# Performance work log

Measured on AMD Instinct MI355X. Metric: run time of the kernel, lower is better.

## Reference

```python
import jax, jax.numpy as jnp
import numpy as np

B, T, D, H, O = 64, 2048, 256, 256, 128


def setup_inputs() -> dict:
    key = jax.random.key(0)
    ks = jax.random.split(key, 12)
    s_in = 1.0 / np.sqrt(H)
    inp = {
        "x": jax.random.normal(ks[0], (B, T, D), dtype=jnp.float32),
        # layer 0 (input_dim -> hidden_dim)
        "W_ih0": jax.random.uniform(ks[1], (H, D), jnp.float32, -s_in, s_in),
        "W_hh0": jax.random.uniform(ks[2], (H, H), jnp.float32, -s_in, s_in),
        "b_ih0": jax.random.uniform(ks[3], (H,), jnp.float32, -s_in, s_in),
        "b_hh0": jax.random.uniform(ks[4], (H,), jnp.float32, -s_in, s_in),
        # layer 1 (hidden_dim -> hidden_dim)
        "W_ih1": jax.random.uniform(ks[5], (H, H), jnp.float32, -s_in, s_in),
        "W_hh1": jax.random.uniform(ks[6], (H, H), jnp.float32, -s_in, s_in),
        "b_ih1": jax.random.uniform(ks[7], (H,), jnp.float32, -s_in, s_in),
        "b_hh1": jax.random.uniform(ks[8], (H,), jnp.float32, -s_in, s_in),
        # final linear
        "fc_w": jax.random.uniform(ks[9], (O, H), jnp.float32, -s_in, s_in),
        "fc_b": jax.random.uniform(ks[10], (O,), jnp.float32, -s_in, s_in),
    }
    return inp


def _rnn_layer(x_tbd, W_ih, W_hh, b_ih, b_hh):
    """x_tbd: [T, B, D_in] -> [T, B, H]. h_t = relu(x_t W_ih^T + b_ih + h_{t-1} W_hh^T + b_hh)."""
    # precompute input projection for all timesteps (one big GEMM)
    xp = jnp.einsum('tbd,hd->tbh', x_tbd, W_ih) + (b_ih + b_hh)

    def step(h, xp_t):
        h = jax.nn.relu(xp_t + h @ W_hh.T)
        return h, h

    h0 = jnp.zeros((x_tbd.shape[1], W_hh.shape[0]), dtype=x_tbd.dtype)
    _, hs = jax.lax.scan(step, h0, xp)
    return hs


def reference(x, W_ih0, W_hh0, b_ih0, b_hh0, W_ih1, W_hh1, b_ih1, b_hh1, fc_w, fc_b):
    x_tbd = jnp.transpose(x, (1, 0, 2))           # [T, B, D]
    h1 = _rnn_layer(x_tbd, W_ih0, W_hh0, b_ih0, b_hh0)   # [T, B, H]
    h2 = _rnn_layer(h1, W_ih1, W_hh1, b_ih1, b_hh1)      # [T, B, H]
    last = h2[-1]                                  # out[:, -1, :] -> [B, H]
    return last @ fc_w.T + fc_b                    # [B, O]
```

## Files before the change

kernel.cpp:

```cpp
#include <hip/hip_runtime.h>
#include <hip/hip_bf16.h>
#include <stdint.h>


typedef float    f32x4  __attribute__((ext_vector_type(4)));
typedef short    s16x8  __attribute__((ext_vector_type(8)));
typedef uint32_t u32x2  __attribute__((ext_vector_type(2)));
typedef uint32_t u32x4v __attribute__((ext_vector_type(4)));

#define T_STEPS 2048

template<bool C, class A, class B> struct cond_ { using type = A; };
template<class A, class B> struct cond_<false, A, B> { using type = B; };

static __device__ __forceinline__ ushort f2bf(float f) {
  uint32_t u = __builtin_bit_cast(uint32_t, f);
  u += 0x7fffu + ((u >> 16) & 1u);
  return (ushort)(u >> 16);
}
static __device__ __forceinline__ float bf2f(ushort h) {
  return __builtin_bit_cast(float, (uint32_t)h << 16);
}
static __device__ __forceinline__ uint32_t packbf(float lo, float hi) {
  return (uint32_t)f2bf(lo) | ((uint32_t)f2bf(hi) << 16);
}
static __device__ __forceinline__ s16x8 pack8(float4 a, float4 b) {
  u32x4v u;
  u.x = packbf(a.x, a.y); u.y = packbf(a.z, a.w);
  u.z = packbf(b.x, b.y); u.w = packbf(b.z, b.w);
  return __builtin_bit_cast(s16x8, u);
}
struct hl2 { uint32_t hi, lo; };
static __device__ __forceinline__ hl2 split2(float a, float b) {
  const ushort ha = f2bf(a), hb = f2bf(b);
  const ushort la = f2bf(a - bf2f(ha)), lb = f2bf(b - bf2f(hb));
  hl2 r;
  r.hi = (uint32_t)ha | ((uint32_t)hb << 16);
  r.lo = (uint32_t)la | ((uint32_t)lb << 16);
  return r;
}
static __device__ __forceinline__ f32x4 expand16(u32x2 p) {
  f32x4 r;
  r.x = __builtin_bit_cast(float, p.x << 16);
  r.y = __builtin_bit_cast(float, p.x & 0xffff0000u);
  r.z = __builtin_bit_cast(float, p.y << 16);
  r.w = __builtin_bit_cast(float, p.y & 0xffff0000u);
  return r;
}
static __device__ __forceinline__ f32x4 acc_of(f32x4 v) { return v; }
static __device__ __forceinline__ f32x4 acc_of(u32x2 v) { return expand16(v); }

#define MFMA16(a, b, c) __builtin_amdgcn_mfma_f32_16x16x32_bf16((a), (b), (c), 0, 0, 0)

template<int MODE, bool XP16>
__global__ __launch_bounds__(256, 2)
void proj_kernel(const void* __restrict__ inp, const float* __restrict__ W,
                 const float* __restrict__ ba, const float* __restrict__ bb,
                 void* __restrict__ xp)
{
  const int tid = threadIdx.x;
  const int w = tid >> 6, lane = tid & 63, q = lane >> 4, r = lane & 15;

  s16x8 wf[4][8];
  float bs[4];
#pragma unroll
  for (int n = 0; n < 4; ++n) {
    const int j = 16 * (4 * w + n) + r;
    bs[n] = ba[j] + bb[j];
    const float* wr = W + (size_t)j * 256 + 8 * q;
#pragma unroll
    for (int c = 0; c < 8; ++c) {
      const float4 f0 = *(const float4*)(wr + 32 * c);
      const float4 f1 = *(const float4*)(wr + 32 * c + 4);
      wf[n][c] = pack8(f0, f1);
    }
  }

  const int t0 = blockIdx.x * 8;
  for (int tt = 0; tt < 8; ++tt) {
    const int t = t0 + tt;
    for (int bg = 0; bg < 4; ++bg) {
      s16x8 af[8];
      if (MODE == 1) {
        const unsigned char* hsl = (const unsigned char*)inp
            + (size_t)t * 32768 + (size_t)bg * 8192 + lane * 16;
#pragma unroll
        for (int c = 0; c < 8; ++c)
          af[c] = __builtin_bit_cast(s16x8, *(const u32x4v*)(hsl + c * 1024));
      } else {
        const float* arow = (const float*)inp + ((size_t)(16 * bg + r) * 2048 + t) * 256 + 8 * q;
#pragma unroll
        for (int c = 0; c < 8; ++c) {
          const float4 f0 = *(const float4*)(arow + 32 * c);
          const float4 f1 = *(const float4*)(arow + 32 * c + 4);
          af[c] = pack8(f0, f1);
        }
      }
      f32x4 a0 = {bs[0], bs[0], bs[0], bs[0]};
      f32x4 a1 = {bs[1], bs[1], bs[1], bs[1]};
      f32x4 a2 = {bs[2], bs[2], bs[2], bs[2]};
      f32x4 a3 = {bs[3], bs[3], bs[3], bs[3]};
#pragma unroll
      for (int c = 0; c < 8; ++c) {
        a0 = MFMA16(af[c], wf[0][c], a0);
        a1 = MFMA16(af[c], wf[1][c], a1);
        a2 = MFMA16(af[c], wf[2][c], a2);
        a3 = MFMA16(af[c], wf[3][c], a3);
      }
      const int ob = (t * 4 + bg) * 1024 + (4 * w) * 64 + lane;
      if constexpr (XP16) {
        u32x2* const xpo = (u32x2*)xp;
        u32x2 s0, s1, s2, s3;
        s0.x = packbf(a0.x, a0.y); s0.y = packbf(a0.z, a0.w);
        s1.x = packbf(a1.x, a1.y); s1.y = packbf(a1.z, a1.w);
        s2.x = packbf(a2.x, a2.y); s2.y = packbf(a2.z, a2.w);
        s3.x = packbf(a3.x, a3.y); s3.y = packbf(a3.z, a3.w);
        xpo[ob +   0] = s0;
        xpo[ob +  64] = s1;
        xpo[ob + 128] = s2;
        xpo[ob + 192] = s3;
      } else {
        f32x4* const xpo = (f32x4*)xp;
        xpo[ob +   0] = a0;
        xpo[ob +  64] = a1;
        xpo[ob + 128] = a2;
        xpo[ob + 192] = a3;
      }
    }
  }
}

template<int LAYER, bool XP16>
__global__ __launch_bounds__(256, 1)
void recur_kernel(const void* __restrict__ xp, const float* __restrict__ Whh,
                  char* __restrict__ h1out, const float* __restrict__ fcw,
                  const float* __restrict__ fcb, float* __restrict__ out)
{
  using XPT = typename cond_<XP16, u32x2, f32x4>::type;
  const int tid = threadIdx.x;
  const int w = tid >> 6, lane = tid & 63, q = lane >> 4, r = lane & 15;
  const int bg = blockIdx.x;

  __shared__ __align__(16) unsigned char smem[16384];

  s16x8 whi[4][8], wlo[4][8];
#pragma unroll
  for (int n = 0; n < 4; ++n) {
    const float* wr = Whh + (size_t)(16 * (4 * w + n) + r) * 256 + 8 * q;
#pragma unroll
    for (int c = 0; c < 8; ++c) {
      const float4 f0 = *(const float4*)(wr + 32 * c);
      const float4 f1 = *(const float4*)(wr + 32 * c + 4);
      const hl2 p0 = split2(f0.x, f0.y);
      const hl2 p1 = split2(f0.z, f0.w);
      const hl2 p2 = split2(f1.x, f1.y);
      const hl2 p3 = split2(f1.z, f1.w);
      u32x4v H, L;
      H.x = p0.hi; L.x = p0.lo;
      H.y = p1.hi; L.y = p1.lo;
      H.z = p2.hi; L.z = p2.lo;
      H.w = p3.hi; L.w = p3.lo;
      whi[n][c] = __builtin_bit_cast(s16x8, H);
      wlo[n][c] = __builtin_bit_cast(s16x8, L);
    }
  }

  {
    uint32_t* z = (uint32_t*)smem;
#pragma unroll
    for (int i = 0; i < 16; ++i) z[tid + 256 * i] = 0u;
  }
  __syncthreads();

  const XPT* __restrict__ xpv = (const XPT*)xp;
  const int xpbase = bg * 1024 + (4 * w) * 64 + lane;

  XPT pfA[4], pfB[4];
#pragma unroll
  for (int n = 0; n < 4; ++n) {
    pfA[n] = xpv[xpbase + n * 64];
    pfB[n] = xpv[4096 + xpbase + n * 64];
  }

  int rb[4];
#pragma unroll
  for (int n = 0; n < 4; ++n) {
    const int k0 = 64 * w + 16 * n + r;
    rb[n] = (k0 >> 5) * 1024 + ((k0 >> 3) & 3) * 256 + (4 * q) * 16 + (k0 & 7) * 2;
  }
  const int rdoff = lane * 16;

#define RSTEP(T_, RD_, WR_, PF_) do {                                           \
    u32x4v afr[8];                                                              \
    _Pragma("unroll")                                                           \
    for (int c = 0; c < 8; ++c)                                                 \
      afr[c] = *(const u32x4v*)(smem + (RD_) + c * 1024 + rdoff);               \
    if (LAYER == 0 && w == 0 && (T_) > 0) {                                     \
      char* hb = h1out + (size_t)((T_) - 1) * 32768 + (size_t)bg * 8192 + rdoff;\
      _Pragma("unroll")                                                         \
      for (int c = 0; c < 8; ++c) *(u32x4v*)(hb + c * 1024) = afr[c];           \
    }                                                                           \
    f32x4 ac0 = acc_of(PF_[0]), ac1 = acc_of(PF_[1]);                           \
    f32x4 ac2 = acc_of(PF_[2]), ac3 = acc_of(PF_[3]);                           \
    { int tp = (T_) + 2; if (tp > T_STEPS - 1) tp = T_STEPS - 1;                \
      const int xo = tp * 4096 + xpbase;                                        \
      PF_[0] = xpv[xo]; PF_[1] = xpv[xo + 64];                                  \
      PF_[2] = xpv[xo + 128]; PF_[3] = xpv[xo + 192]; }                         \
    _Pragma("unroll")                                                           \
    for (int c = 0; c < 8; ++c) {                                               \
      const s16x8 a = __builtin_bit_cast(s16x8, afr[c]);                        \
      ac0 = MFMA16(a, whi[0][c], ac0); ac1 = MFMA16(a, whi[1][c], ac1);         \
      ac2 = MFMA16(a, whi[2][c], ac2); ac3 = MFMA16(a, whi[3][c], ac3);         \
      ac0 = MFMA16(a, wlo[0][c], ac0); ac1 = MFMA16(a, wlo[1][c], ac1);         \
      ac2 = MFMA16(a, wlo[2][c], ac2); ac3 = MFMA16(a, wlo[3][c], ac3);         \
    }                                                                           \
    unsigned char* const wb = smem + (WR_);                                     \
    *(ushort*)(wb + rb[0] +  0) = f2bf(fmaxf(ac0.x, 0.f));                      \
    *(ushort*)(wb + rb[0] + 16) = f2bf(fmaxf(ac0.y, 0.f));                      \
    *(ushort*)(wb + rb[0] + 32) = f2bf(fmaxf(ac0.z, 0.f));                      \
    *(ushort*)(wb + rb[0] + 48) = f2bf(fmaxf(ac0.w, 0.f));                      \
    *(ushort*)(wb + rb[1] +  0) = f2bf(fmaxf(ac1.x, 0.f));                      \
    *(ushort*)(wb + rb[1] + 16) = f2bf(fmaxf(ac1.y, 0.f));                      \
    *(ushort*)(wb + rb[1] + 32) = f2bf(fmaxf(ac1.z, 0.f));                      \
    *(ushort*)(wb + rb[1] + 48) = f2bf(fmaxf(ac1.w, 0.f));                      \
    *(ushort*)(wb + rb[2] +  0) = f2bf(fmaxf(ac2.x, 0.f));                      \
    *(ushort*)(wb + rb[2] + 16) = f2bf(fmaxf(ac2.y, 0.f));                      \
    *(ushort*)(wb + rb[2] + 32) = f2bf(fmaxf(ac2.z, 0.f));                      \
    *(ushort*)(wb + rb[2] + 48) = f2bf(fmaxf(ac2.w, 0.f));                      \
    *(ushort*)(wb + rb[3] +  0) = f2bf(fmaxf(ac3.x, 0.f));                      \
    *(ushort*)(wb + rb[3] + 16) = f2bf(fmaxf(ac3.y, 0.f));                      \
    *(ushort*)(wb + rb[3] + 32) = f2bf(fmaxf(ac3.z, 0.f));                      \
    *(ushort*)(wb + rb[3] + 48) = f2bf(fmaxf(ac3.w, 0.f));                      \
    __syncthreads();                                                            \
  } while (0)

  for (int t = 0; t < T_STEPS; t += 2) {
    RSTEP(t,     0,    8192, pfA);
    RSTEP(t + 1, 8192, 0,    pfB);
  }
#undef RSTEP

  if (LAYER == 0 && w == 0) {
    char* hb = h1out + (size_t)2047 * 32768 + (size_t)bg * 8192 + rdoff;
#pragma unroll
    for (int c = 0; c < 8; ++c)
      *(u32x4v*)(hb + c * 1024) = *(const u32x4v*)(smem + c * 1024 + rdoff);
  }

  if (LAYER == 1) {
    const int m  = tid >> 4;
    const int og = tid & 15;
    float a8[8];
#pragma unroll
    for (int oo = 0; oo < 8; ++oo) a8[oo] = fcb[og * 8 + oo];
    for (int c = 0; c < 8; ++c) {
#pragma unroll
      for (int qq = 0; qq < 4; ++qq) {
        const u32x4v hv = *(const u32x4v*)(smem + c * 1024 + (16 * qq + m) * 16);
        float hf[8];
        hf[0] = bf2f((ushort)(hv.x & 0xffff)); hf[1] = bf2f((ushort)(hv.x >> 16));
        hf[2] = bf2f((ushort)(hv.y & 0xffff)); hf[3] = bf2f((ushort)(hv.y >> 16));
        hf[4] = bf2f((ushort)(hv.z & 0xffff)); hf[5] = bf2f((ushort)(hv.z >> 16));
        hf[6] = bf2f((ushort)(hv.w & 0xffff)); hf[7] = bf2f((ushort)(hv.w >> 16));
        const int kb = 32 * c + 8 * qq;
#pragma unroll
        for (int oo = 0; oo < 8; ++oo) {
          const float* fw = fcw + (size_t)(og * 8 + oo) * 256 + kb;
          const float4 g0 = *(const float4*)(fw);
          const float4 g1 = *(const float4*)(fw + 4);
          a8[oo] += hf[0] * g0.x + hf[1] * g0.y + hf[2] * g0.z + hf[3] * g0.w
                  + hf[4] * g1.x + hf[5] * g1.y + hf[6] * g1.z + hf[7] * g1.w;
        }
      }
    }
#pragma unroll
    for (int oo = 0; oo < 8; ++oo)
      out[(16 * bg + m) * 128 + og * 8 + oo] = a8[oo];
  }
}

extern "C" void kernel_launch(void* const* d_in, const int* in_sizes, int n_in,
                              void* d_out, int out_size, void* d_ws, size_t ws_size,
                              hipStream_t stream) {
  (void)in_sizes; (void)n_in; (void)out_size;
  const float* x     = (const float*)d_in[0];
  const float* W_ih0 = (const float*)d_in[1];
  const float* W_hh0 = (const float*)d_in[2];
  const float* b_ih0 = (const float*)d_in[3];
  const float* b_hh0 = (const float*)d_in[4];
  const float* W_ih1 = (const float*)d_in[5];
  const float* W_hh1 = (const float*)d_in[6];
  const float* b_ih1 = (const float*)d_in[7];
  const float* b_hh1 = (const float*)d_in[8];
  const float* fcw   = (const float*)d_in[9];
  const float* fcb   = (const float*)d_in[10];

  const bool big = ws_size >= (size_t)201326592;
  if (big) {
    void* xp = d_ws;
    char* h1 = (char*)d_ws + (size_t)134217728;
    proj_kernel<0, false><<<256, 256, 0, stream>>>(x, W_ih0, b_ih0, b_hh0, xp);
    recur_kernel<0, false><<<4, 256, 0, stream>>>(xp, W_hh0, h1, nullptr, nullptr, nullptr);
    proj_kernel<1, false><<<256, 256, 0, stream>>>(h1, W_ih1, b_ih1, b_hh1, xp);
    recur_kernel<1, false><<<4, 256, 0, stream>>>(xp, W_hh1, nullptr, fcw, fcb, (float*)d_out);
  } else {
    void* xp = d_ws;
    char* h1 = (char*)d_ws + (size_t)67108864;
    proj_kernel<0, true><<<256, 256, 0, stream>>>(x, W_ih0, b_ih0, b_hh0, xp);
    recur_kernel<0, true><<<4, 256, 0, stream>>>(xp, W_hh0, h1, nullptr, nullptr, nullptr);
    proj_kernel<1, true><<<256, 256, 0, stream>>>(h1, W_ih1, b_ih1, b_hh1, xp);
    recur_kernel<1, true><<<4, 256, 0, stream>>>(xp, W_hh1, nullptr, fcw, fcb, (float*)d_out);
  }
}
```

Baseline: 4.615 ms.

## Swap MFMA operand order so recurrent outputs store as packed bf16 vectors

Swaps the A and B operands of the MFMAs in both the projection and recurrent kernels. Each lane's accumulator then holds four consecutive hidden units for one batch row instead of four batch rows for one unit. In the recurrent step this lets each lane convert its outputs with the hardware packed bf16 convert and write them to LDS as four 8-byte stores, replacing sixteen 2-byte stores. The step sits on the serial critical path, so fewer LDS stores and conversions per step should help. The bias is now loaded per lane as a vector. The projection output layout changes as a consequence, so it must stay consistent with how the recurrent kernel reads xp.

```diff
diff --git a/kernel.cpp b/kernel.cpp
--- a/kernel.cpp
+++ b/kernel.cpp
@@ -23,6 +23,11 @@
 }
 static __device__ __forceinline__ uint32_t packbf(float lo, float hi) {
   return (uint32_t)f2bf(lo) | ((uint32_t)f2bf(hi) << 16);
+}
+static __device__ __forceinline__ uint32_t cvtpk(float lo, float hi) {
+  uint32_t d;
+  asm("v_cvt_pk_bf16_f32 %0, %1, %2" : "=v"(d) : "v"(lo), "v"(hi));
+  return d;
 }
 static __device__ __forceinline__ s16x8 pack8(float4 a, float4 b) {
   u32x4v u;
@@ -62,11 +67,15 @@
   const int w = tid >> 6, lane = tid & 63, q = lane >> 4, r = lane & 15;
 
   s16x8 wf[4][8];
-  float bs[4];
+  f32x4 bs4[4];
 #pragma unroll
   for (int n = 0; n < 4; ++n) {
+    const int j0 = 16 * (4 * w + n) + 4 * q;
+    const float4 b0 = *(const float4*)(ba + j0);
+    const float4 b1 = *(const float4*)(bb + j0);
+    bs4[n].x = b0.x + b1.x; bs4[n].y = b0.y + b1.y;
+    bs4[n].z = b0.z + b1.z; bs4[n].w = b0.w + b1.w;
     const int j = 16 * (4 * w + n) + r;
-    bs[n] = ba[j] + bb[j];
     const float* wr = W + (size_t)j * 256 + 8 * q;
 #pragma unroll
     for (int c = 0; c < 8; ++c) {
@@ -96,16 +105,16 @@
           af[c] = pack8(f0, f1);
         }
       }
-      f32x4 a0 = {bs[0], bs[0], bs[0], bs[0]};
-      f32x4 a1 = {bs[1], bs[1], bs[1], bs[1]};
-      f32x4 a2 = {bs[2], bs[2], bs[2], bs[2]};
-      f32x4 a3 = {bs[3], bs[3], bs[3], bs[3]};
+      f32x4 a0 = bs4[0];
+      f32x4 a1 = bs4[1];
+      f32x4 a2 = bs4[2];
+      f32x4 a3 = bs4[3];
 #pragma unroll
       for (int c = 0; c < 8; ++c) {
-        a0 = MFMA16(af[c], wf[0][c], a0);
-        a1 = MFMA16(af[c], wf[1][c], a1);
-        a2 = MFMA16(af[c], wf[2][c], a2);
-        a3 = MFMA16(af[c], wf[3][c], a3);
+        a0 = MFMA16(wf[0][c], af[c], a0);
+        a1 = MFMA16(wf[1][c], af[c], a1);
+        a2 = MFMA16(wf[2][c], af[c], a2);
+        a3 = MFMA16(wf[3][c], af[c], a3);
       }
       const int ob = (t * 4 + bg) * 1024 + (4 * w) * 64 + lane;
       if constexpr (XP16) {
@@ -182,11 +191,11 @@
     pfB[n] = xpv[4096 + xpbase + n * 64];
   }
 
-  int rb[4];
-#pragma unroll
-  for (int n = 0; n < 4; ++n) {
-    const int k0 = 64 * w + 16 * n + r;
-    rb[n] = (k0 >> 5) * 1024 + ((k0 >> 3) & 3) * 256 + (4 * q) * 16 + (k0 & 7) * 2;
+  int wrb[4];
+#pragma unroll
+  for (int nt = 0; nt < 4; ++nt) {
+    const int k0 = 64 * w + 16 * nt + 4 * q;
+    wrb[nt] = (k0 >> 5) * 1024 + ((k0 >> 3) & 3) * 256 + r * 16 + (k0 & 7) * 2;
   }
   const int rdoff = lane * 16;
 
@@ -209,28 +218,26 @@
     _Pragma("unroll")                                                           \
     for (int c = 0; c < 8; ++c) {                                               \
       const s16x8 a = __builtin_bit_cast(s16x8, afr[c]);                        \
-      ac0 = MFMA16(a, whi[0][c], ac0); ac1 = MFMA16(a, whi[1][c], ac1);         \
-      ac2 = MFMA16(a, whi[2][c], ac2); ac3 = MFMA16(a, whi[3][c], ac3);         \
-      ac0 = MFMA16(a, wlo[0][c], ac0); ac1 = MFMA16(a, wlo[1][c], ac1);         \
-      ac2 = MFMA16(a, wlo[2][c], ac2); ac3 = MFMA16(a, wlo[3][c], ac3);         \
+      ac0 = MFMA16(whi[0][c], a, ac0); ac1 = MFMA16(whi[1][c], a, ac1);         \
+      ac2 = MFMA16(whi[2][c], a, ac2); ac3 = MFMA16(whi[3][c], a, ac3);         \
+      ac0 = MFMA16(wlo[0][c], a, ac0); ac1 = MFMA16(wlo[1][c], a, ac1);         \
+      ac2 = MFMA16(wlo[2][c], a, ac2); ac3 = MFMA16(wlo[3][c], a, ac3);         \
     }                                                                           \
     unsigned char* const wb = smem + (WR_);                                     \
-    *(ushort*)(wb + rb[0] +  0) = f2bf(fmaxf(ac0.x, 0.f));                      \
-    *(ushort*)(wb + rb[0] + 16) = f2bf(fmaxf(ac0.y, 0.f));                      \
-    *(ushort*)(wb + rb[0] + 32) = f2bf(fmaxf(ac0.z, 0.f));                      \
-    *(ushort*)(wb + rb[0] + 48) = f2bf(fmaxf(ac0.w, 0.f));                      \
-    *(ushort*)(wb + rb[1] +  0) = f2bf(fmaxf(ac1.x, 0.f));                      \
-    *(ushort*)(wb + rb[1] + 16) = f2bf(fmaxf(ac1.y, 0.f));                      \
-    *(ushort*)(wb + rb[1] + 32) = f2bf(fmaxf(ac1.z, 0.f));                      \
-    *(ushort*)(wb + rb[1] + 48) = f2bf(fmaxf(ac1.w, 0.f));                      \
-    *(ushort*)(wb + rb[2] +  0) = f2bf(fmaxf(ac2.x, 0.f));                      \
-    *(ushort*)(wb + rb[2] + 16) = f2bf(fmaxf(ac2.y, 0.f));                      \
-    *(ushort*)(wb + rb[2] + 32) = f2bf(fmaxf(ac2.z, 0.f));                      \
-    *(ushort*)(wb + rb[2] + 48) = f2bf(fmaxf(ac2.w, 0.f));                      \
-    *(ushort*)(wb + rb[3] +  0) = f2bf(fmaxf(ac3.x, 0.f));                      \
-    *(ushort*)(wb + rb[3] + 16) = f2bf(fmaxf(ac3.y, 0.f));                      \
-    *(ushort*)(wb + rb[3] + 32) = f2bf(fmaxf(ac3.z, 0.f));                      \
-    *(ushort*)(wb + rb[3] + 48) = f2bf(fmaxf(ac3.w, 0.f));                      \
+    { u32x2 v0, v1, v2, v3;                                                     \
+      v0.x = cvtpk(fmaxf(ac0.x, 0.f), fmaxf(ac0.y, 0.f));                       \
+      v0.y = cvtpk(fmaxf(ac0.z, 0.f), fmaxf(ac0.w, 0.f));                       \
+      v1.x = cvtpk(fmaxf(ac1.x, 0.f), fmaxf(ac1.y, 0.f));                       \
+      v1.y = cvtpk(fmaxf(ac1.z, 0.f), fmaxf(ac1.w, 0.f));                       \
+      v2.x = cvtpk(fmaxf(ac2.x, 0.f), fmaxf(ac2.y, 0.f));                       \
+      v2.y = cvtpk(fmaxf(ac2.z, 0.f), fmaxf(ac2.w, 0.f));                       \
+      v3.x = cvtpk(fmaxf(ac3.x, 0.f), fmaxf(ac3.y, 0.f));                       \
+      v3.y = cvtpk(fmaxf(ac3.z, 0.f), fmaxf(ac3.w, 0.f));                       \
+      *(u32x2*)(wb + wrb[0]) = v0;                                              \
+      *(u32x2*)(wb + wrb[1]) = v1;                                              \
+      *(u32x2*)(wb + wrb[2]) = v2;                                              \
+      *(u32x2*)(wb + wrb[3]) = v3;                                              \
+    }                                                                           \
     __syncthreads();                                                            \
   } while (0)
 
```

New measurement: 4.289 ms. 1.08x faster.
